# Optimization experiments

Measured on AMD Instinct MI355X. Metric: run time of the kernel, lower is better.

## Reference

```python
import jax, jax.numpy as jnp
import numpy as np

N, C, H, W = 32, 24, 14, 14
HD, GH, AS = 128, 256, 28
D_IN = (C + 2) * 2 + HD  # 180


def setup_inputs() -> dict:
    key = jax.random.key(0)
    ks = jax.random.split(key, 10)
    s = 0.05
    inp = {
        "x": jax.random.normal(ks[0], (N, C, H, W), jnp.float32),
        "code": jax.random.normal(ks[1], (N, HD), jnp.float32),
        "gw0": jax.random.normal(ks[2], (D_IN, GH), jnp.float32) * s,
        "gb0": jnp.zeros((GH,), jnp.float32),
        "gw1": jax.random.normal(ks[3], (GH, GH), jnp.float32) * s,
        "gb1": jnp.zeros((GH,), jnp.float32),
        "gw2": jax.random.normal(ks[4], (GH, GH), jnp.float32) * s,
        "gb2": jnp.zeros((GH,), jnp.float32),
        "gw3": jax.random.normal(ks[5], (GH, GH), jnp.float32) * s,
        "gb3": jnp.zeros((GH,), jnp.float32),
        "fw0": jax.random.normal(ks[6], (GH, GH), jnp.float32) * s,
        "fb0": jnp.zeros((GH,), jnp.float32),
        "fw1": jax.random.normal(ks[7], (GH, GH), jnp.float32) * s,
        "fb1": jnp.zeros((GH,), jnp.float32),
        "fw2": jax.random.normal(ks[8], (GH, AS), jnp.float32) * s,
        "fb2": jnp.zeros((AS,), jnp.float32),
    }
    return inp


def _rn_encode(x, code):
    n, c, h, w = x.shape
    o = h * w
    hd = code.shape[1]
    # coordinates: torch.linspace(-h/2, h/2, h) over row dim, (-w/2, w/2, w) over col dim
    xs = jnp.linspace(-h / 2.0, h / 2.0, h, dtype=jnp.float32)
    ys = jnp.linspace(-w / 2.0, w / 2.0, w, dtype=jnp.float32)
    coord = jnp.stack(
        [jnp.broadcast_to(xs[:, None], (h, w)).reshape(o),
         jnp.broadcast_to(ys[None, :], (h, w)).reshape(o)], axis=-1)  # (o, 2)
    feats = x.reshape(n, c, o).transpose(0, 2, 1)  # (n, o, c)
    feats = jnp.concatenate([feats, jnp.broadcast_to(coord, (n, o, 2))], axis=-1)  # (n, o, c+2)
    # pairs[n, i, j] = [feats[n, j], feats[n, i], code[n]]  (matches torch expand semantics)
    p1 = jnp.broadcast_to(feats[:, None, :, :], (n, o, o, c + 2))
    p2 = jnp.broadcast_to(feats[:, :, None, :], (n, o, o, c + 2))
    q = jnp.broadcast_to(code[:, None, None, :], (n, o, o, hd))
    return jnp.concatenate([p1, p2, q], axis=-1).reshape(n, o * o, -1)


def reference(x, code, gw0, gb0, gw1, gb1, gw2, gb2, gw3, gb3,
              fw0, fb0, fw1, fb1, fw2, fb2):
    pairs = _rn_encode(x, code)  # (n, o^2, 180)
    h1 = jax.nn.relu(pairs @ gw0 + gb0)
    h1 = jax.nn.relu(h1 @ gw1 + gb1)
    h1 = jax.nn.relu(h1 @ gw2 + gb2)
    h1 = jax.nn.relu(h1 @ gw3 + gb3)
    relations = h1.sum(axis=1)  # (n, GH) sum-pool over all pairs
    r = jax.nn.relu(relations @ fw0 + fb0)
    r = jax.nn.relu(r @ fw1 + fb1)
    logits = r @ fw2 + fb2  # last layer linear (last=True)
    return logits
```

## Files before the change

kernel.cpp:

```cpp
#include <hip/hip_runtime.h>
#include <hip/hip_bf16.h>


typedef __attribute__((ext_vector_type(8))) short short8;
typedef __attribute__((ext_vector_type(16))) float f32x16;

#define NIMG 32
#define O 196
#define PAIRS 38416
#define GH 256
#define AS 28
#define ROWS 64
#define CHUNKS 601

#define SWZ(row) ((((row) & 7) << 4) ^ (((row) & 8) << 2))

static __device__ __forceinline__ unsigned short f2bf(float f) {
    __hip_bfloat16 h = __float2bfloat16(f);
    return *reinterpret_cast<unsigned short*>(&h);
}

__global__ void k_cc(const float* __restrict__ code, const float* __restrict__ gw0,
                     const float* __restrict__ gb0, float* __restrict__ CC) {
    const int n = blockIdx.x, g = threadIdx.x;
    __shared__ float cs[128];
    if (g < 128) cs[g] = code[n * 128 + g];
    __syncthreads();
    float acc = gb0[g];
    for (int k = 0; k < 128; ++k) acc = fmaf(cs[k], gw0[(52 + k) * GH + g], acc);
    CC[n * GH + g] = acc;
}

__global__ void k_ajbi(const float* __restrict__ x, const float* __restrict__ gw0,
                       const float* __restrict__ CC,
                       float* __restrict__ AJ, float* __restrict__ BI) {
    const int np = blockIdx.x;
    const int n = np / O, p = np - n * O;
    const int g = threadIdx.x;
    __shared__ float fs[26];
    if (g < 24)       fs[g]  = x[(n * 24 + g) * O + p];
    else if (g == 24) fs[24] = -7.0f + (float)(p / 14) * (14.0f / 13.0f);
    else if (g == 25) fs[25] = -7.0f + (float)(p % 14) * (14.0f / 13.0f);
    __syncthreads();
    float aj = CC[n * GH + g], bi = 0.f;
#pragma unroll
    for (int c = 0; c < 26; ++c) {
        const float f = fs[c];
        aj = fmaf(f, gw0[c * GH + g], aj);
        bi = fmaf(f, gw0[(26 + c) * GH + g], bi);
    }
    AJ[np * GH + g] = aj;
    BI[np * GH + g] = bi;
}

__global__ void k_pack(const float* __restrict__ gw1, const float* __restrict__ gw2,
                       const float* __restrict__ gw3, unsigned short* __restrict__ pW) {
    const int idx = blockIdx.x * 256 + threadIdx.x;
    const int L = idx >> 16;
    const int rem = idx & 0xFFFF;
    const int e = rem & 7;
    const int lane = (rem >> 3) & 63;
    const int ks = (rem >> 9) & 15;
    const int nt = rem >> 13;
    const int k = ks * 16 + ((lane >> 5) << 3) + e;
    const int col = nt * 32 + (lane & 31);
    const float* W = (L == 0) ? gw1 : (L == 1) ? gw2 : gw3;
    pW[idx] = f2bf(W[k * GH + col]);
}

__global__ __launch_bounds__(512, 4) void k_main(
    const float* __restrict__ AJ, const float* __restrict__ BI,
    const unsigned short* __restrict__ pW,
    const float* __restrict__ gb1, const float* __restrict__ gb2,
    const float* __restrict__ gb3, float* __restrict__ rel) {
    __shared__ __attribute__((aligned(16))) unsigned short hA[ROWS * GH];
    __shared__ __attribute__((aligned(16))) unsigned short hB[ROWS * GH];

    const int blk = blockIdx.x;
    const int n = blk / CHUNKS;
    const int chunk = blk - n * CHUNKS;
    const int row_base = chunk * ROWS;
    const int t = threadIdx.x;
    const int wave = t >> 6;
    const int lane = t & 63;
    const int l31 = lane & 31;
    const int hi = lane >> 5;
    const int l15 = lane & 15;
    const bool tail = (chunk == CHUNKS - 1);

    {
        const int i0 = row_base / O;
        const int j00 = row_base - i0 * O;
        const int i1 = min(i0 + 1, O - 1);
        const float4 bi0 = *(const float4*)&BI[(n * O + i0) * GH + lane * 4];
        const float4 bi1 = *(const float4*)&BI[(n * O + i1) * GH + lane * 4];
#pragma unroll
        for (int e = 0; e < 8; ++e) {
            const int r = wave + e * 8;
            const int jj = j00 + r;
            const bool wrap = (jj >= O);
            const int j = wrap ? jj - O : jj;
            const float4 aj = *(const float4*)&AJ[(n * O + j) * GH + lane * 4];
            const float4 bi = wrap ? bi1 : bi0;
            const unsigned int lo = (unsigned)f2bf(fmaxf(aj.x + bi.x, 0.f)) |
                                    ((unsigned)f2bf(fmaxf(aj.y + bi.y, 0.f)) << 16);
            const unsigned int hh = (unsigned)f2bf(fmaxf(aj.z + bi.z, 0.f)) |
                                    ((unsigned)f2bf(fmaxf(aj.w + bi.w, 0.f)) << 16);
            const int byteoff = r * 512 + ((lane * 8) ^ SWZ(r));
            uint2 dd; dd.x = lo; dd.y = hh;
            *(uint2*)((char*)hA + byteoff) = dd;
        }
    }
    __syncthreads();

    const int X = SWZ(l15);
    const int hi16 = hi << 4;
    const int arow = l31 * 512;

    auto kloop = [&](const unsigned short* bufR, const short8* wp,
                     f32x16& a0, f32x16& a1, bool swapped) {
        short8 wa = wp[lane], wb = wp[64 + lane], wc = wp[128 + lane], wd = wp[192 + lane];
        const char* hb = (const char*)bufR + arow;
#pragma unroll
        for (int ks = 0; ks < 16; ++ks) {
            const short8 W = (ks & 3) == 0 ? wa : (ks & 3) == 1 ? wb
                           : (ks & 3) == 2 ? wc : wd;
            const int off = (ks * 32 + hi16) ^ X;
            const short8 h0 = *(const short8*)(hb + off);
            const short8 h1 = *(const short8*)(hb + off + 16384);
            if (swapped) {
                a0 = __builtin_amdgcn_mfma_f32_32x32x16_bf16(W, h0, a0, 0, 0, 0);
                a1 = __builtin_amdgcn_mfma_f32_32x32x16_bf16(W, h1, a1, 0, 0, 0);
            } else {
                a0 = __builtin_amdgcn_mfma_f32_32x32x16_bf16(h0, W, a0, 0, 0, 0);
                a1 = __builtin_amdgcn_mfma_f32_32x32x16_bf16(h1, W, a1, 0, 0, 0);
            }
            if (ks < 12) {
                const short8 nw = wp[(ks + 4) * 64 + lane];
                if ((ks & 3) == 0) wa = nw; else if ((ks & 3) == 1) wb = nw;
                else if ((ks & 3) == 2) wc = nw; else wd = nw;
            }
        }
    };

    auto epi = [&](const f32x16& a0, const f32x16& a1, const float* gb,
                   unsigned short* bufW) {
        const float4 b40 = *(const float4*)&gb[wave * 32 + 0  + 4 * hi];
        const float4 b41 = *(const float4*)&gb[wave * 32 + 8  + 4 * hi];
        const float4 b42 = *(const float4*)&gb[wave * 32 + 16 + 4 * hi];
        const float4 b43 = *(const float4*)&gb[wave * 32 + 24 + 4 * hi];
        const float bias[16] = {b40.x, b40.y, b40.z, b40.w, b41.x, b41.y, b41.z, b41.w,
                                b42.x, b42.y, b42.z, b42.w, b43.x, b43.y, b43.z, b43.w};
        char* w0 = (char*)bufW + l31 * 512;
#pragma unroll
        for (int rp = 0; rp < 8; ++rp) {
            const int r0 = rp * 2;
            const float ba = bias[(r0 >> 2) * 4 + (r0 & 3)];
            const float bb = bias[(r0 >> 2) * 4 + (r0 & 3) + 1];
            const int cw = (r0 & 3) + 8 * (r0 >> 2);
            const int cb = (wave * 64 + cw * 2 + hi * 8) ^ X;
            const unsigned p0 = (unsigned)f2bf(fmaxf(a0[r0] + ba, 0.f)) |
                                ((unsigned)f2bf(fmaxf(a0[r0 + 1] + bb, 0.f)) << 16);
            const unsigned p1 = (unsigned)f2bf(fmaxf(a1[r0] + ba, 0.f)) |
                                ((unsigned)f2bf(fmaxf(a1[r0 + 1] + bb, 0.f)) << 16);
            *(unsigned*)(w0 + cb) = p0;
            *(unsigned*)(w0 + 16384 + cb) = p1;
        }
    };

    const f32x16 z = {0.f,0.f,0.f,0.f,0.f,0.f,0.f,0.f,0.f,0.f,0.f,0.f,0.f,0.f,0.f,0.f};
    const short8* wpb = (const short8*)pW + wave * 1024;

    f32x16 acc0 = z, acc1 = z;
    kloop(hA, wpb, acc0, acc1, true);
    epi(acc0, acc1, gb1, hB);
    __syncthreads();

    acc0 = z; acc1 = z;
    kloop(hB, wpb + 8192, acc0, acc1, true);
    epi(acc0, acc1, gb2, hA);
    __syncthreads();

    acc0 = z; acc1 = z;
    kloop(hA, wpb + 16384, acc0, acc1, false);
    {
        const float bias = gb3[wave * 32 + l31];
        float s = 0.f;
        if (!tail) {
#pragma unroll
            for (int r = 0; r < 16; ++r)
                s += fmaxf(acc0[r] + bias, 0.f) + fmaxf(acc1[r] + bias, 0.f);
        } else {
#pragma unroll
            for (int r = 0; r < 8; ++r)
                s += fmaxf(acc0[r] + bias, 0.f);
        }
        s += __shfl_xor(s, 32);
        if (hi == 0) atomicAdd(&rel[n * GH + wave * 32 + l31], s);
    }
}

__global__ void k_fmlp(const float* __restrict__ rel,
                       const float* __restrict__ fw0, const float* __restrict__ fb0,
                       const float* __restrict__ fw1, const float* __restrict__ fb1,
                       const float* __restrict__ fw2, const float* __restrict__ fb2,
                       float* __restrict__ out) {
    __shared__ float b0[GH], b1[GH];
    const int n = blockIdx.x, g = threadIdx.x;
    b0[g] = rel[n * GH + g];
    __syncthreads();
    float a = fb0[g];
    for (int k = 0; k < GH; ++k) a = fmaf(b0[k], fw0[k * GH + g], a);
    b1[g] = fmaxf(a, 0.f);
    __syncthreads();
    float c = fb1[g];
    for (int k = 0; k < GH; ++k) c = fmaf(b1[k], fw1[k * GH + g], c);
    b0[g] = fmaxf(c, 0.f);
    __syncthreads();
    if (g < AS) {
        float o = fb2[g];
        for (int k = 0; k < GH; ++k) o = fmaf(b0[k], fw2[k * AS + g], o);
        out[n * AS + g] = o;
    }
}

extern "C" void kernel_launch(void* const* d_in, const int* in_sizes, int n_in,
                              void* d_out, int out_size, void* d_ws, size_t ws_size,
                              hipStream_t stream) {
    const float* x    = (const float*)d_in[0];
    const float* code = (const float*)d_in[1];
    const float* gw0  = (const float*)d_in[2];
    const float* gb0  = (const float*)d_in[3];
    const float* gw1  = (const float*)d_in[4];
    const float* gb1  = (const float*)d_in[5];
    const float* gw2  = (const float*)d_in[6];
    const float* gb2  = (const float*)d_in[7];
    const float* gw3  = (const float*)d_in[8];
    const float* gb3  = (const float*)d_in[9];
    const float* fw0  = (const float*)d_in[10];
    const float* fb0  = (const float*)d_in[11];
    const float* fw1  = (const float*)d_in[12];
    const float* fb1  = (const float*)d_in[13];
    const float* fw2  = (const float*)d_in[14];
    const float* fb2  = (const float*)d_in[15];
    float* out = (float*)d_out;

    char* ws = (char*)d_ws;
    float*          AJ  = (float*)(ws + 0);
    float*          BI  = (float*)(ws + 6422528);
    float*          CC  = (float*)(ws + 12845056);
    float*          rel = (float*)(ws + 12877824);
    unsigned short* pW  = (unsigned short*)(ws + 12910592);

    hipMemsetAsync(rel, 0, NIMG * GH * sizeof(float), stream);
    k_cc<<<NIMG, 256, 0, stream>>>(code, gw0, gb0, CC);
    k_ajbi<<<NIMG * O, 256, 0, stream>>>(x, gw0, CC, AJ, BI);
    k_pack<<<768, 256, 0, stream>>>(gw1, gw2, gw3, pW);
    k_main<<<NIMG * CHUNKS, 512, 0, stream>>>(AJ, BI, pW, gb1, gb2, gb3, rel);
    k_fmlp<<<NIMG, 256, 0, stream>>>(rel, fw0, fb0, fw1, fb1, fw2, fb2, out);
}
```

Baseline: 593.2 us.

## Single-buffer LDS activations, raise occupancy, add MFMA priority hints

Replaces the two 32KB ping-pong LDS activation buffers with a single buffer. An extra barrier is added between each layer's K-loop and its epilogue write-back so the buffer can be reused in place. Launch bounds are raised from 4 to 6 blocks per CU to use the freed LDS, and the LDS swizzle is changed to a simple XOR on the low 4 row bits. s_setprio is wrapped around the MFMA pairs to favour matrix issue across waves. The cost is one extra block-wide sync per layer and tighter register limits, which risks spills.

```diff
diff --git a/kernel.cpp b/kernel.cpp
--- a/kernel.cpp
+++ b/kernel.cpp
@@ -13,7 +13,7 @@
 #define ROWS 64
 #define CHUNKS 601
 
-#define SWZ(row) ((((row) & 7) << 4) ^ (((row) & 8) << 2))
+#define SWZ16(row) (((row) & 15) << 4)
 
 static __device__ __forceinline__ unsigned short f2bf(float f) {
     __hip_bfloat16 h = __float2bfloat16(f);
@@ -68,13 +68,12 @@
     pW[idx] = f2bf(W[k * GH + col]);
 }
 
-__global__ __launch_bounds__(512, 4) void k_main(
+__global__ __launch_bounds__(512, 6) void k_main(
     const float* __restrict__ AJ, const float* __restrict__ BI,
     const unsigned short* __restrict__ pW,
     const float* __restrict__ gb1, const float* __restrict__ gb2,
     const float* __restrict__ gb3, float* __restrict__ rel) {
-    __shared__ __attribute__((aligned(16))) unsigned short hA[ROWS * GH];
-    __shared__ __attribute__((aligned(16))) unsigned short hB[ROWS * GH];
+    __shared__ __attribute__((aligned(16))) unsigned short h[ROWS * GH];
 
     const int blk = blockIdx.x;
     const int n = blk / CHUNKS;
@@ -106,21 +105,20 @@
                                     ((unsigned)f2bf(fmaxf(aj.y + bi.y, 0.f)) << 16);
             const unsigned int hh = (unsigned)f2bf(fmaxf(aj.z + bi.z, 0.f)) |
                                     ((unsigned)f2bf(fmaxf(aj.w + bi.w, 0.f)) << 16);
-            const int byteoff = r * 512 + ((lane * 8) ^ SWZ(r));
+            const int byteoff = r * 512 + ((lane * 8) ^ SWZ16(r));
             uint2 dd; dd.x = lo; dd.y = hh;
-            *(uint2*)((char*)hA + byteoff) = dd;
-        }
-    }
-    __syncthreads();
-
-    const int X = SWZ(l15);
+            *(uint2*)((char*)h + byteoff) = dd;
+        }
+    }
+    __syncthreads();
+
+    const int X = SWZ16(l15);
     const int hi16 = hi << 4;
     const int arow = l31 * 512;
 
-    auto kloop = [&](const unsigned short* bufR, const short8* wp,
-                     f32x16& a0, f32x16& a1, bool swapped) {
+    auto kloop = [&](const short8* wp, f32x16& a0, f32x16& a1, bool swapped) {
         short8 wa = wp[lane], wb = wp[64 + lane], wc = wp[128 + lane], wd = wp[192 + lane];
-        const char* hb = (const char*)bufR + arow;
+        const char* hb = (const char*)h + arow;
 #pragma unroll
         for (int ks = 0; ks < 16; ++ks) {
             const short8 W = (ks & 3) == 0 ? wa : (ks & 3) == 1 ? wb
@@ -128,6 +126,7 @@
             const int off = (ks * 32 + hi16) ^ X;
             const short8 h0 = *(const short8*)(hb + off);
             const short8 h1 = *(const short8*)(hb + off + 16384);
+            __builtin_amdgcn_s_setprio(1);
             if (swapped) {
                 a0 = __builtin_amdgcn_mfma_f32_32x32x16_bf16(W, h0, a0, 0, 0, 0);
                 a1 = __builtin_amdgcn_mfma_f32_32x32x16_bf16(W, h1, a1, 0, 0, 0);
@@ -135,6 +134,7 @@
                 a0 = __builtin_amdgcn_mfma_f32_32x32x16_bf16(h0, W, a0, 0, 0, 0);
                 a1 = __builtin_amdgcn_mfma_f32_32x32x16_bf16(h1, W, a1, 0, 0, 0);
             }
+            __builtin_amdgcn_s_setprio(0);
             if (ks < 12) {
                 const short8 nw = wp[(ks + 4) * 64 + lane];
                 if ((ks & 3) == 0) wa = nw; else if ((ks & 3) == 1) wb = nw;
@@ -143,15 +143,14 @@
         }
     };
 
-    auto epi = [&](const f32x16& a0, const f32x16& a1, const float* gb,
-                   unsigned short* bufW) {
+    auto epi = [&](const f32x16& a0, const f32x16& a1, const float* gb) {
         const float4 b40 = *(const float4*)&gb[wave * 32 + 0  + 4 * hi];
         const float4 b41 = *(const float4*)&gb[wave * 32 + 8  + 4 * hi];
         const float4 b42 = *(const float4*)&gb[wave * 32 + 16 + 4 * hi];
         const float4 b43 = *(const float4*)&gb[wave * 32 + 24 + 4 * hi];
         const float bias[16] = {b40.x, b40.y, b40.z, b40.w, b41.x, b41.y, b41.z, b41.w,
                                 b42.x, b42.y, b42.z, b42.w, b43.x, b43.y, b43.z, b43.w};
-        char* w0 = (char*)bufW + l31 * 512;
+        char* w0 = (char*)h + l31 * 512;
 #pragma unroll
         for (int rp = 0; rp < 8; ++rp) {
             const int r0 = rp * 2;
@@ -172,17 +171,19 @@
     const short8* wpb = (const short8*)pW + wave * 1024;
 
     f32x16 acc0 = z, acc1 = z;
-    kloop(hA, wpb, acc0, acc1, true);
-    epi(acc0, acc1, gb1, hB);
+    kloop(wpb, acc0, acc1, true);
+    __syncthreads();
+    epi(acc0, acc1, gb1);
     __syncthreads();
 
     acc0 = z; acc1 = z;
-    kloop(hB, wpb + 8192, acc0, acc1, true);
-    epi(acc0, acc1, gb2, hA);
+    kloop(wpb + 8192, acc0, acc1, true);
+    __syncthreads();
+    epi(acc0, acc1, gb2);
     __syncthreads();
 
     acc0 = z; acc1 = z;
-    kloop(hA, wpb + 16384, acc0, acc1, false);
+    kloop(wpb + 16384, acc0, acc1, false);
     {
         const float bias = gb3[wave * 32 + l31];
         float s = 0.f;
```

Measured after the change: 631.6 us. 6.5% more time.
